# Performance work log

Measured on AMD Instinct MI355X. Metric: run time of the kernel, lower is better.

## Reference

```python
import jax, jax.numpy as jnp
import numpy as np

N, M = 100000, 800000
F_IN, F_E, H = 64, 16, 64
T_NODE, T_EDGE = 2, 3
HEAD_DIM = 16.0


def setup_inputs() -> dict:
    key = jax.random.key(0)
    ks = jax.random.split(key, 16)
    inp = {
        "x": jax.random.normal(ks[0], (N, F_IN), jnp.float32),
        "edge_feat": jax.random.normal(ks[1], (M, F_E), jnp.float32),
        "node_type": jax.random.randint(ks[2], (N,), 0, T_NODE, jnp.int32),
        "edge_src": jax.random.randint(ks[3], (M,), 0, N, jnp.int32),
        "edge_dst": jax.random.randint(ks[4], (M,), 0, N, jnp.int32),
        "edge_type": jax.random.randint(ks[5], (M,), 0, T_EDGE, jnp.int32),
    }
    s_n = 1.0 / np.sqrt(F_IN)
    s_e = 1.0 / np.sqrt(F_E)
    for i, name in enumerate(["W1", "W2", "W3", "W4"]):
        inp[name] = jax.random.normal(ks[6 + i], (T_NODE, F_IN, H), jnp.float32) * s_n
        inp["b" + name[1]] = jax.random.normal(ks[10 + i], (T_NODE, H), jnp.float32) * 0.01
    inp["W5"] = jax.random.normal(ks[14], (T_EDGE, F_E, H), jnp.float32) * s_e
    inp["b5"] = jax.random.normal(ks[15], (T_EDGE, H), jnp.float32) * 0.01
    return inp


def _node_proj(x, W, b, node_type):
    # per-node-type linear: [T,F,H] weights, select row per node type
    p = jnp.einsum('nf,tfh->tnh', x, W) + b[:, None, :]      # [T,N,H]
    return jnp.take_along_axis(p, node_type[None, :, None], axis=0)[0]  # [N,H]


def reference(x, edge_feat, W1, b1, W2, b2, W3, b3, W4, b4, W5, b5,
              node_type, edge_src, edge_dst, edge_type):
    n = x.shape[0]
    h1 = _node_proj(x, W1, b1, node_type)
    h2 = _node_proj(x, W2, b2, node_type)
    h3 = _node_proj(x, W3, b3, node_type)
    h4 = _node_proj(x, W4, b4, node_type)
    # per-edge-type linear via weight gather (F_E is small)
    w5e = jnp.einsum('mf,mfh->mh', edge_feat, W5[edge_type]) + b5[edge_type]  # [M,H]
    # scalar attention logit per edge (w3_i . (w4_j + w5_ij)) / sqrt(head_dim)
    num = jnp.sum(h3[edge_dst] * (h4[edge_src] + w5e), axis=-1)  # [M]
    # softmax over a single scalar per edge == 1.0 exactly (faithful to source)
    score = jax.nn.softmax((num / jnp.sqrt(HEAD_DIM))[:, None], axis=-1)[:, 0]  # [M]
    msg = score[:, None] * (h2[edge_src] + w5e)                  # [M,H]
    out = h1 + jax.ops.segment_sum(msg, edge_dst, num_segments=n)
    return out
```

## Files before the change

### kernel.cpp

```cpp
#include <hip/hip_runtime.h>


#define CAP 16
#define OVF_CAP 32768

typedef __attribute__((ext_vector_type(8))) short short8;
typedef __attribute__((ext_vector_type(4))) float f32x4;

__device__ __forceinline__ float b2f(unsigned short u) {
    union { unsigned v; float f; } x; x.v = ((unsigned)u) << 16; return x.f;
}
__device__ __forceinline__ unsigned short f2b(float f) {
    union { float f; unsigned v; } x; x.f = f;
    unsigned u = x.v;
    unsigned r = (u + 0x7FFFu + ((u >> 16) & 1u)) >> 16;
    return (unsigned short)r;
}

__global__ __launch_bounds__(256) void k1a_gemm(
    const float* __restrict__ x, const int* __restrict__ nt,
    const unsigned short* __restrict__ wtb,
    const float* __restrict__ b1, const float* __restrict__ b2,
    float* __restrict__ out, unsigned short* __restrict__ h2b,
    int N)
{
    __shared__ __align__(16) unsigned short sx[128 * 72];
    __shared__ int snt[128];

    int tid = threadIdx.x;
    int rowbase = blockIdx.x * 128;

    if (tid < 128) {
        int r = rowbase + tid;
        snt[tid] = (r < N) ? nt[r] : 0;
    }

    int fr = (tid & 15) * 4;
    int ir = tid >> 4;
#pragma unroll
    for (int it = 0; it < 8; ++it) {
        int i = it * 16 + ir;
        int r = rowbase + i;
        float4 v = make_float4(0.f, 0.f, 0.f, 0.f);
        if (r < N) v = *(const float4*)&x[(size_t)r * 64 + fr];
        ushort4 p;
        p.x = f2b(v.x); p.y = f2b(v.y); p.z = f2b(v.z); p.w = f2b(v.w);
        *(ushort4*)&sx[i * 72 + fr] = p;
    }
    __syncthreads();

    int lane = tid & 63;
    int wid  = tid >> 6;
    int q    = lane >> 4;
    int cc   = lane & 15;
    int m0   = wid * 32;

    f32x4 acc[4][2][4];
#pragma unroll
    for (int mm = 0; mm < 4; ++mm)
#pragma unroll
        for (int s = 0; s < 2; ++s)
#pragma unroll
            for (int t = 0; t < 4; ++t)
                acc[mm][s][t] = (f32x4){0.f, 0.f, 0.f, 0.f};

#pragma unroll
    for (int k0 = 0; k0 < 64; k0 += 32) {
        int ko = k0 + q * 8;
        short8 af0 = *(short8*)&sx[(m0 + cc) * 72 + ko];
        short8 af1 = *(short8*)&sx[(m0 + 16 + cc) * 72 + ko];
#pragma unroll
        for (int mm = 0; mm < 4; ++mm)
#pragma unroll
            for (int t = 0; t < 4; ++t) {
                short8 bf = *(const short8*)
                    &wtb[mm * 4096 + (t * 16 + cc) * 64 + ko];
                acc[mm][0][t] = __builtin_amdgcn_mfma_f32_16x16x32_bf16(
                    af0, bf, acc[mm][0][t], 0, 0, 0);
                acc[mm][1][t] = __builtin_amdgcn_mfma_f32_16x16x32_bf16(
                    af1, bf, acc[mm][1][t], 0, 0, 0);
            }
    }

    float b1v[2][4], b2v[2][4];
#pragma unroll
    for (int ty = 0; ty < 2; ++ty)
#pragma unroll
        for (int t = 0; t < 4; ++t) {
            b1v[ty][t] = b1[ty * 64 + t * 16 + cc];
            b2v[ty][t] = b2[ty * 64 + t * 16 + cc];
        }

#pragma unroll
    for (int s = 0; s < 2; ++s)
#pragma unroll
        for (int reg = 0; reg < 4; ++reg) {
            int rl_ = m0 + s * 16 + q * 4 + reg;
            int r = rowbase + rl_;
            if (r < N) {
                int ty = snt[rl_];
#pragma unroll
                for (int t = 0; t < 4; ++t) {
                    float v1 = (ty ? acc[1][s][t][reg] : acc[0][s][t][reg])
                               + b1v[ty][t];
                    float v2 = (ty ? acc[3][s][t][reg] : acc[2][s][t][reg])
                               + b2v[ty][t];
                    out[(size_t)r * 64 + t * 16 + cc] = v1;
                    h2b[(size_t)r * 64 + t * 16 + cc] = f2b(v2);
                }
            }
        }
}

__global__ __launch_bounds__(256) void k1b_scatter(
    const int* __restrict__ esrc, const int* __restrict__ edst,
    const int* __restrict__ etype,
    int* __restrict__ cnt32, int* __restrict__ ovfCnt,
    int4* __restrict__ ovf, int2* __restrict__ rec,
    const float* __restrict__ W1, const float* __restrict__ W2,
    unsigned short* __restrict__ wtb,
    int M, int scatterBlocks)
{
    int tid = threadIdx.x;

    if (blockIdx.x == (unsigned)scatterBlocks) {
#pragma unroll
        for (int mm = 0; mm < 4; ++mm) {
            const float* src = ((mm < 2) ? W1 : W2) + (mm & 1) * 4096;
            for (int idx = tid; idx < 4096; idx += 256) {
                int n = idx >> 6;
                int k = idx & 63;
                wtb[mm * 4096 + n * 64 + k] = f2b(src[k * 64 + n]);
            }
        }
        return;
    }

    int e0 = blockIdx.x * 1024 + tid;
    int dd[4], ssrc[4], tty[4];
    bool v[4];
#pragma unroll
    for (int j = 0; j < 4; ++j) {
        int e = e0 + j * 256;
        v[j] = e < M;
        int ec = v[j] ? e : 0;
        dd[j]   = edst[ec];
        ssrc[j] = esrc[ec];
        tty[j]  = etype[ec];
    }
    int pos[4];
#pragma unroll
    for (int j = 0; j < 4; ++j)
        if (v[j]) pos[j] = atomicAdd(&cnt32[dd[j]], 1);
#pragma unroll
    for (int j = 0; j < 4; ++j) {
        if (!v[j]) continue;
        int packed = ssrc[j] | (tty[j] << 20);
        int e = e0 + j * 256;
        if (pos[j] < CAP) {
            rec[dd[j] * CAP + pos[j]] = make_int2(packed, e);
        } else {
            int slot = atomicAdd(ovfCnt, 1);
            if (slot < OVF_CAP) ovf[slot] = make_int4(packed, e, dd[j], 0);
        }
    }
}

__global__ __launch_bounds__(256) void k2_gather_mm(
    const float* __restrict__ ef, const int2* __restrict__ rec,
    const int* __restrict__ cnt32,
    const float* __restrict__ W5, const float* __restrict__ b5,
    const int4* __restrict__ ovf, const int* __restrict__ ovfCnt,
    const unsigned short* __restrict__ h2b, float* __restrict__ out,
    int N, int gatherBlocks, int ovfBlocks)
{
    __shared__ __align__(16) unsigned short sa[32 * 136];
    __shared__ __align__(16) unsigned short swt[64 * 72];
    __shared__ __align__(16) float sH[32 * 66];
    __shared__ int sCnt[32];

    int tid = threadIdx.x;
    int lane = tid & 63;
    int wid = tid >> 6;

    if (blockIdx.x >= (unsigned)gatherBlocks) {
        int novf = min(*ovfCnt, OVF_CAP);
        int gw = (blockIdx.x - gatherBlocks) * 4 + wid;
        int nw = ovfBlocks * 4;
        for (int ri = gw; ri < novf; ri += nw) {
            int4 o = ovf[ri];
            int s = o.x & 0xFFFFF;
            int t = (unsigned)o.x >> 20;
            float acc = b5[t * 64 + lane] + b2f(h2b[((size_t)s << 6) | lane]);
#pragma unroll
            for (int f = 0; f < 16; ++f)
                acc = fmaf(ef[(size_t)o.y * 16 + f],
                           W5[(t * 16 + f) * 64 + lane], acc);
            unsafeAtomicAdd(&out[(size_t)o.z * 64 + lane], acc);
        }
        return;
    }

#pragma unroll
    for (int k = 0; k < 13; ++k) {
        int idx = tid + k * 256;
        int j = idx >> 6;
        int h = idx & 63;
        float wv = 0.f;
        if (j < 48)      wv = W5[j * 64 + h];
        else if (j < 51) wv = b5[(j - 48) * 64 + h];
        swt[h * 72 + j] = f2b(wv);
    }
    {
        ushort4 z; z.x = 0; z.y = 0; z.z = 0; z.w = 0;
        if (tid < 192) {
            int h = tid / 3;
            int sp = (tid - h * 3) * 4;
            *(ushort4*)&swt[h * 72 + 52 + sp] = z;
        }
        if (tid < 192) {
            int row = tid / 6;
            int w6 = tid - row * 6;
            int sp = (w6 < 3) ? (52 + w6 * 4) : (116 + (w6 - 3) * 4);
            *(ushort4*)&sa[row * 136 + sp] = z;
        }
    }

    int myt = (lane < 48) ? (lane >> 4) : (lane - 48);
    unsigned myf = lane & 15;
    bool fl = lane < 48;
    int wbase = blockIdx.x * 32 + wid * 8;

    int cnts[8];
#pragma unroll
    for (int g = 0; g < 8; ++g) {
        int d = wbase + g;
        cnts[g] = (d < N) ? cnt32[d] : 0;
    }
    if (lane == 0) {
#pragma unroll
        for (int g = 0; g < 8; ++g) sCnt[wid * 8 + g] = cnts[g];
    }

#pragma unroll 1
    for (int gp = 0; gp < 8; gp += 2) {
        int dA = wbase + gp, dB = dA + 1;
        int dgA = min(cnts[gp], CAP);
        int dgB = min(cnts[gp + 1], CAP);
        unsigned baseA = (unsigned)(dA < N ? dA : 0) * CAP;
        unsigned baseB = (unsigned)(dB < N ? dB : 0) * CAP;

        int2 rA[8], rB[8];
#pragma unroll
        for (int j = 0; j < 8; ++j) rA[j] = rec[baseA + j];
#pragma unroll
        for (int j = 0; j < 8; ++j) rB[j] = rec[baseB + j];

        float hvA[8], evA[8], hvB[8], evB[8];
#pragma unroll
        for (int j = 0; j < 8; ++j) {
            bool ok = j < dgA;
            unsigned s = ok ? ((unsigned)rA[j].x & 0xFFFFFu) : 0u;
            unsigned e = ok ? (unsigned)rA[j].y : 0u;
            hvA[j] = b2f(h2b[((size_t)s << 6) | (unsigned)lane]);
            evA[j] = ef[(e << 4) | myf];
        }
#pragma unroll
        for (int j = 0; j < 8; ++j) {
            bool ok = j < dgB;
            unsigned s = ok ? ((unsigned)rB[j].x & 0xFFFFFu) : 0u;
            unsigned e = ok ? (unsigned)rB[j].y : 0u;
            hvB[j] = b2f(h2b[((size_t)s << 6) | (unsigned)lane]);
            evB[j] = ef[(e << 4) | myf];
        }

        float accHA = 0.f, accSA = 0.f, accHB = 0.f, accSB = 0.f;
#pragma unroll
        for (int j = 0; j < 8; ++j) {
            bool okA = j < dgA;
            int tA = (int)((unsigned)rA[j].x >> 20);
            accHA += okA ? hvA[j] : 0.f;
            float vA = fl ? evA[j] : 1.0f;
            accSA += (okA && tA == myt) ? vA : 0.f;
            bool okB = j < dgB;
            int tB = (int)((unsigned)rB[j].x >> 20);
            accHB += okB ? hvB[j] : 0.f;
            float vB = fl ? evB[j] : 1.0f;
            accSB += (okB && tB == myt) ? vB : 0.f;
        }

        if (dgA > 8) {
            int2 r2[8];
#pragma unroll
            for (int j = 0; j < 8; ++j)
                r2[j] = rec[baseA + (unsigned)min(8 + j, dgA - 1)];
#pragma unroll
            for (int j = 0; j < 8; ++j) {
                unsigned s = (unsigned)r2[j].x & 0xFFFFFu;
                float hv = b2f(h2b[((size_t)s << 6) | (unsigned)lane]);
                float evv = ef[((unsigned)r2[j].y << 4) | myf];
                int t = (int)((unsigned)r2[j].x >> 20);
                bool ok = (8 + j) < dgA;
                accHA += ok ? hv : 0.f;
                float v = fl ? evv : 1.0f;
                accSA += (ok && t == myt) ? v : 0.f;
            }
        }
        if (dgB > 8) {
            int2 r2[8];
#pragma unroll
            for (int j = 0; j < 8; ++j)
                r2[j] = rec[baseB + (unsigned)min(8 + j, dgB - 1)];
#pragma unroll
            for (int j = 0; j < 8; ++j) {
                unsigned s = (unsigned)r2[j].x & 0xFFFFFu;
                float hv = b2f(h2b[((size_t)s << 6) | (unsigned)lane]);
                float evv = ef[((unsigned)r2[j].y << 4) | myf];
                int t = (int)((unsigned)r2[j].x >> 20);
                bool ok = (8 + j) < dgB;
                accHB += ok ? hv : 0.f;
                float v = fl ? evv : 1.0f;
                accSB += (ok && t == myt) ? v : 0.f;
            }
        }

        int wdA = wid * 8 + gp, wdB = wdA + 1;
        if (lane < 52) {
            unsigned short hiA = f2b(accSA);
            sa[wdA * 136 + lane] = hiA;
            sa[wdA * 136 + 64 + lane] = f2b(accSA - b2f(hiA));
            unsigned short hiB = f2b(accSB);
            sa[wdB * 136 + lane] = hiB;
            sa[wdB * 136 + 64 + lane] = f2b(accSB - b2f(hiB));
        }
        sH[wdA * 66 + lane] = accHA;
        sH[wdB * 66 + lane] = accHB;
    }
    __syncthreads();

    int q  = lane >> 4;
    int cc = lane & 15;
    int s  = wid & 1;
    int t0 = wid >> 1;

    f32x4 acc0 = (f32x4){0.f, 0.f, 0.f, 0.f};
    f32x4 acc1 = (f32x4){0.f, 0.f, 0.f, 0.f};
#pragma unroll
    for (int k0 = 0; k0 < 128; k0 += 32) {
        int ko = k0 + q * 8;
        int kb = ko & 63;
        short8 af = *(short8*)&sa[(s * 16 + cc) * 136 + ko];
        short8 bf0 = *(short8*)&swt[(t0 * 16 + cc) * 72 + kb];
        short8 bf1 = *(short8*)&swt[((t0 + 2) * 16 + cc) * 72 + kb];
        acc0 = __builtin_amdgcn_mfma_f32_16x16x32_bf16(af, bf0, acc0, 0, 0, 0);
        acc1 = __builtin_amdgcn_mfma_f32_16x16x32_bf16(af, bf1, acc1, 0, 0, 0);
    }

#pragma unroll
    for (int reg = 0; reg < 4; ++reg) {
        int rl = s * 16 + q * 4 + reg;
        int d = blockIdx.x * 32 + rl;
        if (d < N) {
            int c0 = t0 * 16 + cc;
            int c1 = (t0 + 2) * 16 + cc;
            float v0 = acc0[reg] + sH[rl * 66 + c0];
            float v1 = acc1[reg] + sH[rl * 66 + c1];
            float* p0 = &out[(size_t)d * 64 + c0];
            float* p1 = &out[(size_t)d * 64 + c1];
            if (sCnt[rl] > CAP) {
                unsafeAtomicAdd(p0, v0);
                unsafeAtomicAdd(p1, v1);
            } else {
                *p0 += v0;
                *p1 += v1;
            }
        }
    }
}

extern "C" void kernel_launch(void* const* d_in, const int* in_sizes, int n_in,
                              void* d_out, int out_size, void* d_ws, size_t ws_size,
                              hipStream_t stream) {
    const float* x  = (const float*)d_in[0];
    const float* ef = (const float*)d_in[1];
    const int* nt   = (const int*)d_in[2];
    const int* es   = (const int*)d_in[3];
    const int* ed   = (const int*)d_in[4];
    const int* et   = (const int*)d_in[5];
    const float* W1 = (const float*)d_in[6];
    const float* b1 = (const float*)d_in[7];
    const float* W2 = (const float*)d_in[8];
    const float* b2 = (const float*)d_in[9];
    const float* W5 = (const float*)d_in[14];
    const float* b5 = (const float*)d_in[15];

    int N = in_sizes[2];
    int M = in_sizes[3];

    char* w = (char*)d_ws;
    size_t off = 0;
    unsigned short* h2b = (unsigned short*)(w + off); off += (size_t)N * 64 * 2;
    off = (off + 255) & ~(size_t)255;
    int2* rec = (int2*)(w + off); off += (size_t)N * CAP * 8;
    off = (off + 255) & ~(size_t)255;
    int4* ovf = (int4*)(w + off); off += (size_t)OVF_CAP * 16;
    off = (off + 255) & ~(size_t)255;
    unsigned short* wtb = (unsigned short*)(w + off); off += 4 * 4096 * 2;
    off = (off + 255) & ~(size_t)255;
    int* ovfCnt = (int*)(w + off);
    int* cnt32  = (int*)(w + off + 64);
    size_t zeroBytes = 64 + (size_t)N * 4;

    float* out = (float*)d_out;

    hipMemsetAsync(ovfCnt, 0, zeroBytes, stream);

    int scatterBlocks = (M + 1023) / 1024;
    k1b_scatter<<<scatterBlocks + 1, 256, 0, stream>>>(
        es, ed, et, cnt32, ovfCnt, ovf, rec, W1, W2, wtb, M, scatterBlocks);

    int gemmBlocks = (N + 127) / 128;
    k1a_gemm<<<gemmBlocks, 256, 0, stream>>>(
        x, nt, wtb, b1, b2, out, h2b, N);

    int gatherBlocks = (N + 31) / 32;
    int ovfBlocks = 32;
    k2_gather_mm<<<gatherBlocks + ovfBlocks, 256, 0, stream>>>(
        ef, rec, cnt32, W5, b5, ovf, ovfCnt, h2b, out,
        N, gatherBlocks, ovfBlocks);
}
```

Measured before the change: 297.8 us.

## Fuse edge scatter and node GEMM into one interleaved launch; replace memset

```diff
diff --git a/kernel.cpp b/kernel.cpp
--- a/kernel.cpp
+++ b/kernel.cpp
@@ -17,18 +17,72 @@
     return (unsigned short)r;
 }
 
-__global__ __launch_bounds__(256) void k1a_gemm(
+__global__ __launch_bounds__(256) void k0_init(
+    int* __restrict__ zeroBase, int nZero,
+    const float* __restrict__ W1, const float* __restrict__ W2,
+    unsigned short* __restrict__ wtb)
+{
+    int idx = blockIdx.x * 256 + threadIdx.x;
+    if (idx < nZero) zeroBase[idx] = 0;
+    if (idx < 16384) {
+        int mm = idx >> 12;
+        int r  = idx & 4095;
+        int n  = r >> 6;
+        int k  = r & 63;
+        const float* src = ((mm < 2) ? W1 : W2) + (mm & 1) * 4096;
+        wtb[mm * 4096 + n * 64 + k] = f2b(src[k * 64 + n]);
+    }
+}
+
+__global__ __launch_bounds__(256) void k1_fused(
     const float* __restrict__ x, const int* __restrict__ nt,
     const unsigned short* __restrict__ wtb,
     const float* __restrict__ b1, const float* __restrict__ b2,
+    const int* __restrict__ esrc, const int* __restrict__ edst,
+    const int* __restrict__ etype,
+    int* __restrict__ cnt32, int* __restrict__ ovfCnt,
+    int4* __restrict__ ovf, int2* __restrict__ rec,
     float* __restrict__ out, unsigned short* __restrict__ h2b,
-    int N)
+    int N, int M)
 {
     __shared__ __align__(16) unsigned short sx[128 * 72];
     __shared__ int snt[128];
 
     int tid = threadIdx.x;
-    int rowbase = blockIdx.x * 128;
+
+    if (blockIdx.x & 1) {
+        int e0 = (blockIdx.x >> 1) * 1024 + tid;
+        int dd[4], ssrc[4], tty[4];
+        bool v[4];
+#pragma unroll
+        for (int j = 0; j < 4; ++j) {
+            int e = e0 + j * 256;
+            v[j] = e < M;
+            int ec = v[j] ? e : 0;
+            dd[j]   = edst[ec];
+            ssrc[j] = esrc[ec];
+            tty[j]  = etype[ec];
+        }
+        int pos[4];
+#pragma unroll
+        for (int j = 0; j < 4; ++j)
+            if (v[j]) pos[j] = atomicAdd(&cnt32[dd[j]], 1);
+#pragma unroll
+        for (int j = 0; j < 4; ++j) {
+            if (!v[j]) continue;
+            int packed = ssrc[j] | (tty[j] << 20);
+            int e = e0 + j * 256;
+            if (pos[j] < CAP) {
+                rec[dd[j] * CAP + pos[j]] = make_int2(packed, e);
+            } else {
+                int slot = atomicAdd(ovfCnt, 1);
+                if (slot < OVF_CAP) ovf[slot] = make_int4(packed, e, dd[j], 0);
+            }
+        }
+        return;
+    }
+
+    int rowbase = (blockIdx.x >> 1) * 128;
 
     if (tid < 128) {
         int r = rowbase + tid;
@@ -110,60 +164,6 @@
                 }
             }
         }
-}
-
-__global__ __launch_bounds__(256) void k1b_scatter(
-    const int* __restrict__ esrc, const int* __restrict__ edst,
-    const int* __restrict__ etype,
-    int* __restrict__ cnt32, int* __restrict__ ovfCnt,
-    int4* __restrict__ ovf, int2* __restrict__ rec,
-    const float* __restrict__ W1, const float* __restrict__ W2,
-    unsigned short* __restrict__ wtb,
-    int M, int scatterBlocks)
-{
-    int tid = threadIdx.x;
-
-    if (blockIdx.x == (unsigned)scatterBlocks) {
-#pragma unroll
-        for (int mm = 0; mm < 4; ++mm) {
-            const float* src = ((mm < 2) ? W1 : W2) + (mm & 1) * 4096;
-            for (int idx = tid; idx < 4096; idx += 256) {
-                int n = idx >> 6;
-                int k = idx & 63;
-                wtb[mm * 4096 + n * 64 + k] = f2b(src[k * 64 + n]);
-            }
-        }
-        return;
-    }
-
-    int e0 = blockIdx.x * 1024 + tid;
-    int dd[4], ssrc[4], tty[4];
-    bool v[4];
-#pragma unroll
-    for (int j = 0; j < 4; ++j) {
-        int e = e0 + j * 256;
-        v[j] = e < M;
-        int ec = v[j] ? e : 0;
-        dd[j]   = edst[ec];
-        ssrc[j] = esrc[ec];
-        tty[j]  = etype[ec];
-    }
-    int pos[4];
-#pragma unroll
-    for (int j = 0; j < 4; ++j)
-        if (v[j]) pos[j] = atomicAdd(&cnt32[dd[j]], 1);
-#pragma unroll
-    for (int j = 0; j < 4; ++j) {
-        if (!v[j]) continue;
-        int packed = ssrc[j] | (tty[j] << 20);
-        int e = e0 + j * 256;
-        if (pos[j] < CAP) {
-            rec[dd[j] * CAP + pos[j]] = make_int2(packed, e);
-        } else {
-            int slot = atomicAdd(ovfCnt, 1);
-            if (slot < OVF_CAP) ovf[slot] = make_int4(packed, e, dd[j], 0);
-        }
-    }
 }
 
 __global__ __launch_bounds__(256) void k2_gather_mm(
@@ -409,19 +409,19 @@
     off = (off + 255) & ~(size_t)255;
     int* ovfCnt = (int*)(w + off);
     int* cnt32  = (int*)(w + off + 64);
-    size_t zeroBytes = 64 + (size_t)N * 4;
+    int nZero = 16 + N;
 
     float* out = (float*)d_out;
 
-    hipMemsetAsync(ovfCnt, 0, zeroBytes, stream);
-
+    int initBlocks = (nZero + 255) / 256;
+    k0_init<<<initBlocks, 256, 0, stream>>>(ovfCnt, nZero, W1, W2, wtb);
+
+    int gemmBlocks    = (N + 127) / 128;
     int scatterBlocks = (M + 1023) / 1024;
-    k1b_scatter<<<scatterBlocks + 1, 256, 0, stream>>>(
-        es, ed, et, cnt32, ovfCnt, ovf, rec, W1, W2, wtb, M, scatterBlocks);
-
-    int gemmBlocks = (N + 127) / 128;
-    k1a_gemm<<<gemmBlocks, 256, 0, stream>>>(
-        x, nt, wtb, b1, b2, out, h2b, N);
+    int gb1 = 2 * max(gemmBlocks, scatterBlocks);
+    k1_fused<<<gb1, 256, 0, stream>>>(
+        x, nt, wtb, b1, b2, es, ed, et,
+        cnt32, ovfCnt, ovf, rec, out, h2b, N, M);
 
     int gatherBlocks = (N + 31) / 32;
     int ovfBlocks = 32;
```

Result: faster. 279.2 us (-6.2%).
